# Kernel optimization log

Measured on AMD Instinct MI355X. Metric: run time of the kernel, lower is better.

## Reference

```python
import jax, jax.numpy as jnp
import numpy as np

# ---- Cl(4,1) Cayley table (conformal GA: metric +,+,+,+,-) ----
_METRIC = (1.0, 1.0, 1.0, 1.0, -1.0)

def _reorder_sign(a, b):
    # sign from counting swaps to bring blade product to canonical order
    a >>= 1
    s = 0
    while a:
        s += bin(a & b).count("1")
        a >>= 1
    return -1.0 if (s & 1) else 1.0

def _build_cayley():
    C = np.zeros((32, 32, 32), dtype=np.float32)
    for a in range(32):
        for b in range(32):
            s = _reorder_sign(a, b)
            common = a & b
            for i in range(5):
                if (common >> i) & 1:
                    s *= _METRIC[i]
            C[a, b, a ^ b] += s
    return C

CAYLEY = _build_cayley()  # [32,32,32]; out_k = sum_ij C[i,j,k] x_i y_j

EPS = 1e-8

def normalize_cl41(x):
    n = jnp.sqrt(jnp.sum(x * x, axis=-1, keepdims=True))
    return x / (n + EPS)


def setup_inputs() -> dict:
    key = jax.random.key(0)
    k_x, k_wi, k_bi, k_wo, k_bo = jax.random.split(key, 5)
    B, S, D, H = 64, 2048, 6, 8
    x = jax.random.normal(k_x, (B, S, D), dtype=jnp.float32)
    W_in = jax.random.normal(k_wi, (D, H * 32), dtype=jnp.float32) * (1.0 / np.sqrt(D))
    b_in = jax.random.normal(k_bi, (H * 32,), dtype=jnp.float32) * 0.01
    W_out = jax.random.normal(k_wo, (H * 32, 32), dtype=jnp.float32) * (1.0 / np.sqrt(H * 32))
    b_out = jax.random.normal(k_bo, (32,), dtype=jnp.float32) * 0.01
    return {"x": x, "W_in": W_in, "b_in": b_in, "W_out": W_out, "b_out": b_out}


def reference(x, W_in, b_in, W_out, b_out):
    B, S, D = x.shape
    H = W_in.shape[1] // 32
    C = jnp.asarray(CAYLEY)
    # project inputs to per-channel multivectors: (B,S,H,32)
    u = (x @ W_in + b_in).reshape(B, S, H, 32)
    # initial rotor state: identity (scalar blade = 1)
    psi0 = jnp.zeros((B, H, 32), dtype=x.dtype).at[..., 0].set(1.0)

    def step(psi, u_t):  # u_t: (B,H,32)
        delta = normalize_cl41(u_t.at[..., 0].add(1.0))
        psi = normalize_cl41(jnp.einsum("bhi,bhj,ijk->bhk", delta, psi, C))
        return psi, psi

    _, psi_seq = jax.lax.scan(step, psi0, jnp.swapaxes(u, 0, 1))  # (S,B,H,32)
    out = normalize_cl41(psi_seq.reshape(S, B, H * 32) @ W_out + b_out)  # (S,B,32)
    return jnp.swapaxes(out, 0, 1)  # (B,S,32)
```

## Files before the change

kernel.cpp:

```cpp
#include <hip/hip_runtime.h>
#include <hip/hip_bf16.h>
#include <stdint.h>

#define BB 64
#define SS 2048
#define DD 6
#define HH 8
#define NCH 512
#define CHUNKS 256
#define LCH 8

typedef unsigned short ushort_t;
typedef __attribute__((ext_vector_type(8))) __bf16 bf16x8;
typedef __attribute__((ext_vector_type(4))) float f32x4;

#define WAVE_LDS_FENCE() do { \
    asm volatile("s_waitcnt lgkmcnt(0)" ::: "memory"); \
    __builtin_amdgcn_sched_barrier(0); } while (0)

struct SignTab { float s[32][32]; };

constexpr int popc5_c(unsigned v) {
    int c = 0;
    for (int i = 0; i < 5; ++i) c += (v >> i) & 1u;
    return c;
}

constexpr SignTab make_signs() {
    SignTab t{};
    for (int a = 0; a < 32; ++a) {
        for (int b = 0; b < 32; ++b) {
            int cnt = 0;
            unsigned aa = ((unsigned)a) >> 1;
            while (aa) { cnt += popc5_c(aa & (unsigned)b); aa >>= 1; }
            if ((a & b) & 16) cnt += 1;
            t.s[a][b] = (cnt & 1) ? -1.0f : 1.0f;
        }
    }
    return t;
}

constexpr SignTab SGN = make_signs();

__device__ __forceinline__ void gp_cl41(const float* __restrict__ a,
                                        const float* __restrict__ b,
                                        float* __restrict__ o) {
#pragma unroll
    for (int k = 0; k < 32; ++k) o[k] = 0.0f;
#pragma unroll
    for (int i = 0; i < 32; ++i) {
#pragma unroll
        for (int k = 0; k < 32; ++k) {
            o[k] = fmaf(SGN.s[i][i ^ k] * a[i], b[i ^ k], o[k]);
        }
    }
}

__device__ __forceinline__ float sumsq32(const float* v) {
    float n0 = 0.f, n1 = 0.f, n2 = 0.f, n3 = 0.f;
#pragma unroll
    for (int k = 0; k < 32; k += 4) {
        n0 = fmaf(v[k+0], v[k+0], n0);
        n1 = fmaf(v[k+1], v[k+1], n1);
        n2 = fmaf(v[k+2], v[k+2], n2);
        n3 = fmaf(v[k+3], v[k+3], n3);
    }
    return (n0 + n1) + (n2 + n3);
}

__device__ __forceinline__ float rsq(float n) {
    return __builtin_amdgcn_rsqf(n);
}

__device__ __forceinline__ uint32_t f2bf_rne(float f) {
    uint32_t u = __float_as_uint(f);
    return (u + 0x7FFFu + ((u >> 16) & 1u)) >> 16;
}

__device__ __forceinline__ void make_delta2(const float4* __restrict__ sW,
                                            const float* __restrict__ xv,
                                            float* __restrict__ dl0,
                                            float* __restrict__ dl1) {
#pragma unroll
    for (int j4 = 0; j4 < 8; ++j4) {
        float4 bv = sW[48 + j4];
        dl0[4*j4+0] = bv.x; dl0[4*j4+1] = bv.y; dl0[4*j4+2] = bv.z; dl0[4*j4+3] = bv.w;
        dl1[4*j4+0] = bv.x; dl1[4*j4+1] = bv.y; dl1[4*j4+2] = bv.z; dl1[4*j4+3] = bv.w;
    }
#pragma unroll
    for (int d = 0; d < 6; ++d) {
        float a0 = xv[d], a1 = xv[6 + d];
#pragma unroll
        for (int j4 = 0; j4 < 8; ++j4) {
            float4 w = sW[d * 8 + j4];
            dl0[4*j4+0] = fmaf(a0, w.x, dl0[4*j4+0]);
            dl0[4*j4+1] = fmaf(a0, w.y, dl0[4*j4+1]);
            dl0[4*j4+2] = fmaf(a0, w.z, dl0[4*j4+2]);
            dl0[4*j4+3] = fmaf(a0, w.w, dl0[4*j4+3]);
            dl1[4*j4+0] = fmaf(a1, w.x, dl1[4*j4+0]);
            dl1[4*j4+1] = fmaf(a1, w.y, dl1[4*j4+1]);
            dl1[4*j4+2] = fmaf(a1, w.z, dl1[4*j4+2]);
            dl1[4*j4+3] = fmaf(a1, w.w, dl1[4*j4+3]);
        }
    }
    dl0[0] += 1.0f;
    dl1[0] += 1.0f;
}

__device__ __forceinline__ void loadx12(const float* __restrict__ xr, float* __restrict__ xv) {
    const float4* xp = (const float4*)xr;
#pragma unroll
    for (int m = 0; m < 3; ++m) {
        float4 t4 = xp[m];
        xv[4*m] = t4.x; xv[4*m+1] = t4.y; xv[4*m+2] = t4.z; xv[4*m+3] = t4.w;
    }
}

__global__ __launch_bounds__(256, 1) void k_scan(
        const float* __restrict__ x, const float* __restrict__ W_in,
        const float* __restrict__ b_in, float* __restrict__ Ebuf) {
    __shared__ float4 sW4[57];
    __shared__ float sT[CHUNKS][36];

    int chain = blockIdx.x;
    int b = chain >> 3, h = chain & 7;
    int c = threadIdx.x;

    if (c < 56) {
        float4 v;
        if (c < 48) {
            int d = c / 8, j4 = c % 8;
            const float* p = W_in + d * 256 + h * 32 + 4 * j4;
            v = make_float4(p[0], p[1], p[2], p[3]);
        } else {
            const float* p = b_in + h * 32 + 4 * (c - 48);
            v = make_float4(p[0], p[1], p[2], p[3]);
        }
        sW4[c] = v;
    }
    __syncthreads();

    const float* xrow = x + ((size_t)b * SS + (size_t)c * LCH) * DD;
    float P[32], O[32];
    {
        float xv[12];
        loadx12(xrow, xv);
        float dl0[32], dl1[32];
        make_delta2(sW4, xv, dl0, dl1);
        gp_cl41(dl1, dl0, P);
    }
#pragma unroll 1
    for (int pr = 1; pr < 4; ++pr) {
        float xv[12];
        loadx12(xrow + 12 * pr, xv);
        float dl0[32], dl1[32];
        make_delta2(sW4, xv, dl0, dl1);
        gp_cl41(dl0, P, O);
        gp_cl41(dl1, O, P);
    }

    float v[32];
    {
        float inv = rsq(sumsq32(P));
#pragma unroll
        for (int k = 0; k < 32; ++k) v[k] = P[k] * inv;
#pragma unroll
        for (int m = 0; m < 8; ++m)
            *(float4*)&sT[c][4*m] = make_float4(v[4*m], v[4*m+1], v[4*m+2], v[4*m+3]);
    }
    __syncthreads();

    int rr = 0;
#pragma unroll 1
    for (int off = 1; off < 128; off <<= 1, ++rr) {
        float w[32];
        bool act = (c >= off);
        if (act) {
#pragma unroll
            for (int m = 0; m < 8; ++m) {
                float4 t4 = *(const float4*)&sT[c - off][4*m];
                w[4*m] = t4.x; w[4*m+1] = t4.y; w[4*m+2] = t4.z; w[4*m+3] = t4.w;
            }
        }
        __syncthreads();
        if (act) {
            gp_cl41(v, w, O);
            if (rr & 1) {
                float inv = rsq(sumsq32(O));
#pragma unroll
                for (int k = 0; k < 32; ++k) v[k] = O[k] * inv;
            } else {
#pragma unroll
                for (int k = 0; k < 32; ++k) v[k] = O[k];
            }
#pragma unroll
            for (int m = 0; m < 8; ++m)
                *(float4*)&sT[c][4*m] = make_float4(v[4*m], v[4*m+1], v[4*m+2], v[4*m+3]);
        }
        __syncthreads();
    }

    if (c >= 128) {
        float w[32];
#pragma unroll
        for (int m = 0; m < 8; ++m) {
            float4 t4 = *(const float4*)&sT[c - 128][4*m];
            w[4*m] = t4.x; w[4*m+1] = t4.y; w[4*m+2] = t4.z; w[4*m+3] = t4.w;
        }
        gp_cl41(v, w, O);
#pragma unroll
        for (int k = 0; k < 32; ++k) v[k] = O[k];
    }

    float* dst = Ebuf + (size_t)chain * CHUNKS * 32;
    if (c == 0) {
        *(float4*)dst = make_float4(1.f, 0.f, 0.f, 0.f);
#pragma unroll
        for (int m = 1; m < 8; ++m) *(float4*)(dst + 4*m) = make_float4(0.f, 0.f, 0.f, 0.f);
    }
    if (c < CHUNKS - 1) {
        float inv = rsq(sumsq32(v));
        float* d2 = dst + (size_t)(c + 1) * 32;
#pragma unroll
        for (int m = 0; m < 8; ++m)
            *(float4*)(d2 + 4*m) = make_float4(v[4*m] * inv, v[4*m+1] * inv,
                                               v[4*m+2] * inv, v[4*m+3] * inv);
    }
}

__global__ __launch_bounds__(256, 1) void k_chain_proj(
        const float* __restrict__ x, const float* __restrict__ W_in,
        const float* __restrict__ b_in, const float* __restrict__ Ebuf,
        const float* __restrict__ W_out, const float* __restrict__ b_out,
        float* __restrict__ out) {
    __shared__ float4 sW4[8][57];
    __shared__ float sX[1536];
    __shared__ ushort_t Wt[32 * 256];
    __shared__ ushort_t psiT[4 * 16 * 256];

    int tid = threadIdx.x;
    int wv = tid >> 6, lane = tid & 63;
    int b = blockIdx.x >> 3, gq = blockIdx.x & 7;
    int grp = gq * 4 + wv;
    int c0 = grp * 8;
    int cl = lane >> 3, h = lane & 7;
    int q = lane >> 4, n0 = lane & 15;

    float4 pv[8];
    {
        const float4* ep = (const float4*)(Ebuf +
                (((size_t)b * HH + h) * CHUNKS + (c0 + cl)) * 32);
#pragma unroll
        for (int m = 0; m < 8; ++m) pv[m] = ep[m];
    }

    for (int idx = tid; idx < 448; idx += 256) {
        int hh = idx / 56, r = idx % 56;
        float4 v;
        if (r < 48) {
            int d = r / 8, j4 = r % 8;
            const float* p = W_in + d * 256 + hh * 32 + 4 * j4;
            v = make_float4(p[0], p[1], p[2], p[3]);
        } else {
            const float* p = b_in + hh * 32 + 4 * (r - 48);
            v = make_float4(p[0], p[1], p[2], p[3]);
        }
        sW4[hh][r] = v;
    }

    {
        const float4* xp = (const float4*)(x + ((size_t)b * SS + (size_t)gq * 256) * DD);
        float4* sx4 = (float4*)sX;
        for (int idx = tid; idx < 384; idx += 256) sx4[idx] = xp[idx];
    }

    for (int idx = tid; idx < 2048; idx += 256) {
        int k = idx >> 3, n4 = (idx & 7) << 2;
        float4 w4 = ((const float4*)W_out)[idx];
        ushort_t vals[4] = { (ushort_t)f2bf_rne(w4.x), (ushort_t)f2bf_rne(w4.y),
                             (ushort_t)f2bf_rne(w4.z), (ushort_t)f2bf_rne(w4.w) };
#pragma unroll
        for (int j = 0; j < 4; ++j) {
            int n = n4 + j;
            uint32_t off = (uint32_t)(n * 512 + 2 * k) ^ (uint32_t)((n & 7) << 4);
            *(ushort_t*)((char*)Wt + off) = vals[j];
        }
    }
    __syncthreads();

    float p[32];
#pragma unroll
    for (int m = 0; m < 8; ++m) {
        p[4*m] = pv[m].x; p[4*m+1] = pv[m].y; p[4*m+2] = pv[m].z; p[4*m+3] = pv[m].w;
    }

    bf16x8 Bf[2][8];
#pragma unroll
    for (int nt = 0; nt < 2; ++nt) {
        int n = nt * 16 + n0;
        uint32_t rb = (uint32_t)(n * 512);
        uint32_t sw = (uint32_t)((n & 7) << 4);
#pragma unroll
        for (int kk = 0; kk < 8; ++kk)
            Bf[nt][kk] = *(const bf16x8*)((const char*)Wt + ((rb + kk * 64 + q * 16) ^ sw));
    }
    float bn0 = b_out[n0], bn1 = b_out[16 + n0];

    ushort_t* myT = psiT + wv * 16 * 256;

#pragma unroll 1
    for (int pr = 0; pr < 4; ++pr) {
        float xv[12];
        {
            const float* xr = sX + (wv * 64 + cl * 8 + 2 * pr) * 6;
            loadx12(xr, xv);
        }

        float dl0[32], dl1[32], o[32];
        make_delta2(sW4[h], xv, dl0, dl1);

        gp_cl41(dl0, p, o);
        {
            float inv = rsq(sumsq32(o));
            int row = cl * 2;
            uint32_t rb = (uint32_t)(row * 512 + h * 64);
            uint32_t sw = (uint32_t)((row & 7) << 4);
            uint32_t pk[16];
#pragma unroll
            for (int m = 0; m < 16; ++m)
                pk[m] = f2bf_rne(o[2*m] * inv) | (f2bf_rne(o[2*m+1] * inv) << 16);
#pragma unroll
            for (int m = 0; m < 4; ++m)
                *(uint4*)((char*)myT + ((rb + 16 * m) ^ sw)) =
                    make_uint4(pk[4*m], pk[4*m+1], pk[4*m+2], pk[4*m+3]);
        }
        gp_cl41(dl1, o, p);
        {
            float inv = rsq(sumsq32(p));
            int row = cl * 2 + 1;
            uint32_t rb = (uint32_t)(row * 512 + h * 64);
            uint32_t sw = (uint32_t)((row & 7) << 4);
            uint32_t pk[16];
#pragma unroll
            for (int m = 0; m < 16; ++m)
                pk[m] = f2bf_rne(p[2*m] * inv) | (f2bf_rne(p[2*m+1] * inv) << 16);
#pragma unroll
            for (int m = 0; m < 4; ++m)
                *(uint4*)((char*)myT + ((rb + 16 * m) ^ sw)) =
                    make_uint4(pk[4*m], pk[4*m+1], pk[4*m+2], pk[4*m+3]);
        }

        WAVE_LDS_FENCE();

        f32x4 acc0 = {0.f, 0.f, 0.f, 0.f};
        f32x4 acc1 = {0.f, 0.f, 0.f, 0.f};
        {
            uint32_t rb = (uint32_t)(n0 * 512);
            uint32_t sw = (uint32_t)((n0 & 7) << 4);
#pragma unroll
            for (int kk = 0; kk < 8; ++kk) {
                bf16x8 af = *(const bf16x8*)((const char*)myT + ((rb + kk * 64 + q * 16) ^ sw));
                acc0 = __builtin_amdgcn_mfma_f32_16x16x32_bf16(af, Bf[0][kk], acc0, 0, 0, 0);
                acc1 = __builtin_amdgcn_mfma_f32_16x16x32_bf16(af, Bf[1][kk], acc1, 0, 0, 0);
            }
        }

        float c0v[4], c1v[4], ssq[4];
#pragma unroll
        for (int i = 0; i < 4; ++i) {
            c0v[i] = acc0[i] + bn0;
            c1v[i] = acc1[i] + bn1;
            ssq[i] = c0v[i] * c0v[i] + c1v[i] * c1v[i];
        }
#pragma unroll
        for (int m = 1; m < 16; m <<= 1) {
#pragma unroll
            for (int i = 0; i < 4; ++i) ssq[i] += __shfl_xor(ssq[i], m);
        }
#pragma unroll
        for (int i = 0; i < 4; ++i) {
            float inv = rsq(ssq[i]);
            int mrow = q * 4 + i;
            int s = (c0 + (mrow >> 1)) * LCH + 2 * pr + (mrow & 1);
            size_t row = (size_t)b * SS + s;
            out[row * 32 + n0]      = c0v[i] * inv;
            out[row * 32 + 16 + n0] = c1v[i] * inv;
        }

        WAVE_LDS_FENCE();
    }
}

extern "C" void kernel_launch(void* const* d_in, const int* in_sizes, int n_in,
                              void* d_out, int out_size, void* d_ws, size_t ws_size,
                              hipStream_t stream) {
    const float* x     = (const float*)d_in[0];
    const float* W_in  = (const float*)d_in[1];
    const float* b_in  = (const float*)d_in[2];
    const float* W_out = (const float*)d_in[3];
    const float* b_out = (const float*)d_in[4];
    float* out = (float*)d_out;

    float* Ebuf = (float*)d_ws;

    k_scan      <<<NCH, 256, 0, stream>>>(x, W_in, b_in, Ebuf);
    k_chain_proj<<<NCH, 256, 0, stream>>>(x, W_in, b_in, Ebuf, W_out, b_out, out);
}
```

Before: 173.8 us.

## Stream single-step deltas in scan, raise occupancy, drop LDS fences, add MFMA priority

The chunk scan in k_scan now builds one delta at a time instead of pairs, which cuts live registers, and its launch bounds go from 1 to 3 blocks per CU to allow more occupancy. The projection kernel loses its explicit s_waitcnt and sched_barrier fences around the LDS tile and wraps the MFMA loop in s_setprio. Removing the fences relies on the compiler to order the LDS write and read within a wave. If it does not, this risks a race between the packed bf16 writes and the MFMA reads, and the loose scheduling may reorder work.

After: 303.3 us. 1.75x slower.

```diff
diff --git a/kernel.cpp b/kernel.cpp
--- a/kernel.cpp
+++ b/kernel.cpp
@@ -13,10 +13,6 @@
 typedef unsigned short ushort_t;
 typedef __attribute__((ext_vector_type(8))) __bf16 bf16x8;
 typedef __attribute__((ext_vector_type(4))) float f32x4;
-
-#define WAVE_LDS_FENCE() do { \
-    asm volatile("s_waitcnt lgkmcnt(0)" ::: "memory"); \
-    __builtin_amdgcn_sched_barrier(0); } while (0)
 
 struct SignTab { float s[32][32]; };
 
@@ -75,6 +71,29 @@
 __device__ __forceinline__ uint32_t f2bf_rne(float f) {
     uint32_t u = __float_as_uint(f);
     return (u + 0x7FFFu + ((u >> 16) & 1u)) >> 16;
+}
+
+__device__ __forceinline__ void make_delta1(const float4* __restrict__ sW,
+                                            const float* __restrict__ x6,
+                                            float* __restrict__ dl) {
+#pragma unroll
+    for (int j4 = 0; j4 < 8; ++j4) {
+        float4 bv = sW[48 + j4];
+        dl[4*j4+0] = bv.x; dl[4*j4+1] = bv.y; dl[4*j4+2] = bv.z; dl[4*j4+3] = bv.w;
+    }
+#pragma unroll
+    for (int d = 0; d < 6; ++d) {
+        float a = x6[d];
+#pragma unroll
+        for (int j4 = 0; j4 < 8; ++j4) {
+            float4 w = sW[d * 8 + j4];
+            dl[4*j4+0] = fmaf(a, w.x, dl[4*j4+0]);
+            dl[4*j4+1] = fmaf(a, w.y, dl[4*j4+1]);
+            dl[4*j4+2] = fmaf(a, w.z, dl[4*j4+2]);
+            dl[4*j4+3] = fmaf(a, w.w, dl[4*j4+3]);
+        }
+    }
+    dl[0] += 1.0f;
 }
 
 __device__ __forceinline__ void make_delta2(const float4* __restrict__ sW,
@@ -107,6 +126,15 @@
     dl1[0] += 1.0f;
 }
 
+__device__ __forceinline__ void loadx6(const float* __restrict__ xr, float* __restrict__ xv) {
+    const float2* xp = (const float2*)xr;
+#pragma unroll
+    for (int m = 0; m < 3; ++m) {
+        float2 t2 = xp[m];
+        xv[2*m] = t2.x; xv[2*m+1] = t2.y;
+    }
+}
+
 __device__ __forceinline__ void loadx12(const float* __restrict__ xr, float* __restrict__ xv) {
     const float4* xp = (const float4*)xr;
 #pragma unroll
@@ -116,7 +144,7 @@
     }
 }
 
-__global__ __launch_bounds__(256, 1) void k_scan(
+__global__ __launch_bounds__(256, 3) void k_scan(
         const float* __restrict__ x, const float* __restrict__ W_in,
         const float* __restrict__ b_in, float* __restrict__ Ebuf) {
     __shared__ float4 sW4[57];
@@ -141,29 +169,34 @@
     __syncthreads();
 
     const float* xrow = x + ((size_t)b * SS + (size_t)c * LCH) * DD;
-    float P[32], O[32];
+    float P[32], O[32], dl[32];
     {
-        float xv[12];
-        loadx12(xrow, xv);
-        float dl0[32], dl1[32];
-        make_delta2(sW4, xv, dl0, dl1);
-        gp_cl41(dl1, dl0, P);
+        float xv[6];
+        loadx6(xrow, xv);
+        make_delta1(sW4, xv, P);
     }
 #pragma unroll 1
-    for (int pr = 1; pr < 4; ++pr) {
-        float xv[12];
-        loadx12(xrow + 12 * pr, xv);
-        float dl0[32], dl1[32];
-        make_delta2(sW4, xv, dl0, dl1);
-        gp_cl41(dl0, P, O);
-        gp_cl41(dl1, O, P);
+    for (int tp = 0; tp < 3; ++tp) {
+        float xv[6];
+        loadx6(xrow + 6 * (2 * tp + 1), xv);
+        make_delta1(sW4, xv, dl);
+        gp_cl41(dl, P, O);
+        loadx6(xrow + 6 * (2 * tp + 2), xv);
+        make_delta1(sW4, xv, dl);
+        gp_cl41(dl, O, P);
+    }
+    {
+        float xv[6];
+        loadx6(xrow + 42, xv);
+        make_delta1(sW4, xv, dl);
+        gp_cl41(dl, P, O);
     }
 
     float v[32];
     {
-        float inv = rsq(sumsq32(P));
-#pragma unroll
-        for (int k = 0; k < 32; ++k) v[k] = P[k] * inv;
+        float inv = rsq(sumsq32(O));
+#pragma unroll
+        for (int k = 0; k < 32; ++k) v[k] = O[k] * inv;
 #pragma unroll
         for (int m = 0; m < 8; ++m)
             *(float4*)&sT[c][4*m] = make_float4(v[4*m], v[4*m+1], v[4*m+2], v[4*m+3]);
@@ -350,10 +383,9 @@
                     make_uint4(pk[4*m], pk[4*m+1], pk[4*m+2], pk[4*m+3]);
         }
 
-        WAVE_LDS_FENCE();
-
         f32x4 acc0 = {0.f, 0.f, 0.f, 0.f};
         f32x4 acc1 = {0.f, 0.f, 0.f, 0.f};
+        __builtin_amdgcn_s_setprio(1);
         {
             uint32_t rb = (uint32_t)(n0 * 512);
             uint32_t sw = (uint32_t)((n0 & 7) << 4);
@@ -364,6 +396,7 @@
                 acc1 = __builtin_amdgcn_mfma_f32_16x16x32_bf16(af, Bf[1][kk], acc1, 0, 0, 0);
             }
         }
+        __builtin_amdgcn_s_setprio(0);
 
         float c0v[4], c1v[4], ssq[4];
 #pragma unroll
@@ -386,8 +419,6 @@
             out[row * 32 + n0]      = c0v[i] * inv;
             out[row * 32 + 16 + n0] = c1v[i] * inv;
         }
-
-        WAVE_LDS_FENCE();
     }
 }
 
```
